# Optimization experiments

Hardware: AMD Instinct MI355X
Metric: run time of the kernel (lower is better)

The kernel has to match this reference:

```python
import jax, jax.numpy as jnp
import numpy as np

MAX_DIST = 10
FP_PENALTY = 2.0


def _min_dist_to(mask, BIG):
    """Per-position distance to the nearest True in mask along axis 1.

    mask: [B, S] bool. Returns int32 [B, S]; BIG where the row has no True.
    Replaces the O(B*S_switch^2) Python loops with two cummax scans.
    """
    B, S = mask.shape
    idx = jnp.arange(S, dtype=jnp.int32)
    def one_side(m):
        last = jax.lax.cummax(jnp.where(m, idx, jnp.int32(-BIG)), axis=1)
        return idx - last  # distance to nearest True at or before each position
    d_fwd = one_side(mask)
    d_bwd = jnp.flip(one_side(jnp.flip(mask, axis=1)), axis=1)
    return jnp.minimum(jnp.minimum(d_fwd, d_bwd), BIG)


def setup_inputs() -> dict:
    key = jax.random.key(0)
    k1, k2 = jax.random.split(key)
    B, S, C = 256, 32768, 3
    logits = jax.random.normal(k1, (B, S, C), dtype=jnp.float32)
    labels = jax.random.randint(k2, (B, S), 0, 3, dtype=jnp.int32)
    distance_weights = jnp.array(
        [1.0, 0.99, 0.95, 0.9, 0.85, 0.8, 0.75, 0.7, 0.65, 0.6, 0.55], jnp.float32)
    class_weights = jnp.array([1.0, 10.0, 10.0], jnp.float32)
    return {"logits": logits, "labels": labels,
            "distance_weights": distance_weights, "class_weights": class_weights}


def reference(logits, labels, distance_weights, class_weights):
    B, S, C = logits.shape
    BIG = 2 * S

    valid = labels != -100
    safe_labels = jnp.where(valid, labels, 0)

    # weighted CE, reduction='none', ignore_index=-100
    logp = jax.nn.log_softmax(logits, axis=-1)
    nll = -jnp.take_along_axis(logp, safe_labels[..., None], axis=-1)[..., 0]
    ce = jnp.where(valid, nll * class_weights[safe_labels], 0.0)

    switch = (labels == 1) | (labels == 2)          # true switch positions
    preds = jnp.argmax(logits, axis=-1)
    pred_switch = (preds == 1) | (preds == 2)       # predicted switch positions

    d_to_true = _min_dist_to(switch, BIG)           # nearest true switch per position
    d_to_pred = _min_dist_to(pred_switch, BIG)      # nearest predicted switch per position

    validf = valid.astype(ce.dtype)

    # proximity bonus at valid predicted-switch positions near a true switch
    n_w = distance_weights.shape[0]
    w = jnp.take(distance_weights, jnp.clip(d_to_true, 0, n_w - 1))
    bonus_mask = pred_switch & valid & (d_to_true <= MAX_DIST)
    bonus = jnp.where(bonus_mask, ce * w * 0.5, 0.0)

    # double CE at valid true switches far from every predicted switch
    # (torch code skips this entirely when the row has no predicted switch)
    has_pred = jnp.any(pred_switch, axis=1, keepdims=True)
    double_mask = switch & valid & has_pred & (d_to_pred > MAX_DIST)
    ce = jnp.where(double_mask, ce * 2.0, ce) - bonus

    masked = ce * validf
    fp = pred_switch.astype(ce.dtype) * (1.0 - switch.astype(ce.dtype)) * validf * FP_PENALTY
    total = masked + fp
    return total.sum() / jnp.maximum(validf.sum(), 1.0)
```

## Files before the change

kernel.cpp:

```cpp
#include <hip/hip_runtime.h>
#include <stdint.h>

#define MAX_DIST 10
#define FP_PENALTY 2.0f
#define CHUNK 4096
#define NT 512
#define PPT (CHUNK / NT)
#define NG 2
#define GP 4
#define NBYTES (CHUNK / 8 + 4)
#define NDW ((NBYTES + 3) / 4)

__global__ __launch_bounds__(NT, 6) void pal_main(
    const float* __restrict__ logits, const int* __restrict__ labels,
    const float* __restrict__ dw, const float* __restrict__ cw,
    double* __restrict__ blk_base, double* __restrict__ blk_extra,
    int* __restrict__ blk_valid, int* __restrict__ blk_haspred,
    int S, int chunks_per_row)
{
    __shared__ unsigned int swb32[NDW];
    __shared__ unsigned int psb32[NDW];
    __shared__ float tbl[12];
    __shared__ float rb[NT / 64], rex[NT / 64];
    __shared__ int rvfp[NT / 64], rp[NT / 64];

    unsigned char* swb = (unsigned char*)swb32;
    unsigned char* psb = (unsigned char*)psb32;

    const int t = threadIdx.x;
    const int wave = t >> 6, lane = t & 63;
    const int blk = blockIdx.x;
    const int row = blk / chunks_per_row;
    const int ck  = blk % chunks_per_row;
    const int s0  = ck * CHUNK;
    const long long rowbase = (long long)row * S;
    const long long pbase = rowbase + s0 + (long long)t * PPT;

    if (t < 12) tbl[t] = (t < 11) ? 0.5f * dw[t] : 0.0f;
    const float cw0 = cw[0], cw1 = cw[1], cw2 = cw[2];

    int4   lb[NG];
    float4 x0[NG], x1[NG], x2[NG];
    #pragma unroll
    for (int g = 0; g < NG; ++g) {
        lb[g] = *(const int4*)(labels + pbase + g * GP);
        const float* lp = logits + (pbase + g * GP) * 3;
        x0[g] = *(const float4*)(lp);
        x1[g] = *(const float4*)(lp + 4);
        x2[g] = *(const float4*)(lp + 8);
    }
    __builtin_amdgcn_sched_barrier(0);

    float ce[PPT];
    unsigned swm = 0u, psm = 0u, vvm = 0u;
    #pragma unroll
    for (int g = 0; g < NG; ++g) {
        const float L[12] = { x0[g].x, x0[g].y, x0[g].z, x0[g].w,
                              x1[g].x, x1[g].y, x1[g].z, x1[g].w,
                              x2[g].x, x2[g].y, x2[g].z, x2[g].w };
        const int lbl4[4] = { lb[g].x, lb[g].y, lb[g].z, lb[g].w };
        #pragma unroll
        for (int i = 0; i < GP; ++i) {
            const int j = g * GP + i;
            const int lbl = lbl4[i];
            const float l0 = L[3*i], l1 = L[3*i+1], l2 = L[3*i+2];

            int pred = 0; float best = l0;
            if (l1 > best) { best = l1; pred = 1; }
            if (l2 > best) { best = l2; pred = 2; }

            const bool valid = (lbl != -100);
            const int sl = valid ? lbl : 0;
            const float a = (pred == 0) ? l1 : l0;
            const float b = (pred == 2) ? l1 : l2;
            const float esum = 1.0f + __expf(a - best) + __expf(b - best);
            const float lse = best + __logf(esum);
            const float lt  = (sl == 0) ? l0 : (sl == 1 ? l1 : l2);
            const float cwv = (sl == 0) ? cw0 : (sl == 1 ? cw1 : cw2);
            ce[j] = valid ? (lse - lt) * cwv : 0.0f;

            swm |= ((lbl == 1) || (lbl == 2)) ? (1u << j) : 0u;
            psm |= (pred != 0) ? (1u << j) : 0u;
            vvm |= valid ? (1u << j) : 0u;
        }
    }
    swb[t + 2] = (unsigned char)swm;
    psb[t + 2] = (unsigned char)psm;
    const int vfp = __popc(vvm) | (__popc(psm & ~swm & vvm) << 16);
    const bool anyp = (psm != 0u);

    if (wave == 0) {
        bool sw = false, ps = false;
        int s = -1;
        if (lane < 10) s = s0 - 10 + lane;
        else if (lane >= 32 && lane < 42) s = s0 + CHUNK + (lane - 32);
        if (s >= 0 && s < S) {
            const long long g = rowbase + s;
            const int lbl = labels[g];
            const float* lp = logits + g * 3;
            const float l0 = lp[0], l1 = lp[1], l2 = lp[2];
            int pred = 0; float best = l0;
            if (l1 > best) { best = l1; pred = 1; }
            if (l2 > best) { best = l2; pred = 2; }
            sw = (lbl == 1) || (lbl == 2);
            ps = (pred == 1) || (pred == 2);
        }
        const unsigned long long bs = __ballot(sw ? 1 : 0);
        const unsigned long long bp = __ballot(ps ? 1 : 0);
        if (lane == 0) {
            *(unsigned short*)&swb[0] = (unsigned short)((bs & 0x3FFull) << 6);
            *(unsigned short*)&psb[0] = (unsigned short)((bp & 0x3FFull) << 6);
            *(unsigned short*)&swb[CHUNK / 8 + 2] = (unsigned short)((bs >> 32) & 0x3FFull);
            *(unsigned short*)&psb[CHUNK / 8 + 2] = (unsigned short)((bp >> 32) & 0x3FFull);
        }
    }
    __syncthreads();

    const int di = t >> 2;
    const int off = ((t & 3) << 3) + 6;
    const unsigned sext = __builtin_amdgcn_alignbit(swb32[di + 1], swb32[di], off);
    const unsigned pext = __builtin_amdgcn_alignbit(psb32[di + 1], psb32[di], off);

    float base_acc = 0.0f, extra_acc = 0.0f;
    #pragma unroll
    for (int j = 0; j < PPT; ++j) {
        const unsigned swin = (sext >> j) & 0x1FFFFFu;
        const unsigned pwin = (pext >> j) & 0x1FFFFFu;

        const bool sw_self = (swin >> 10) & 1u;
        const bool ps_self = (pwin >> 10) & 1u;
        const bool npnear  = (pwin == 0u);

        const unsigned low10 = swin & 0x3FFu;
        const unsigned up10  = (swin >> 11) & 0x3FFu;
        const int ddown = __clz((low10 << 21) | 0x100000u);
        const int dup   = __ffs(up10 | 0x400u);
        int dt = min(ddown, dup);
        dt = sw_self ? 0 : dt;

        const float f = ps_self ? tbl[dt] : 0.0f;
        base_acc += ce[j] * (1.0f - f);
        extra_acc += (sw_self && npnear) ? ce[j] : 0.0f;
    }

    float ba = base_acc, ea = extra_acc; int vf = vfp;
    for (int offr = 32; offr; offr >>= 1) {
        ba += __shfl_down(ba, offr);
        ea += __shfl_down(ea, offr);
        vf += __shfl_down(vf, offr);
    }
    const bool wave_any = __any(anyp ? 1 : 0);
    if (lane == 0) {
        rb[wave] = ba; rex[wave] = ea; rvfp[wave] = vf; rp[wave] = wave_any ? 1 : 0;
    }
    __syncthreads();
    if (t == 0) {
        double bsum = 0.0, esum = 0.0; int vs = 0, fps = 0, ap = 0;
        for (int i = 0; i < NT / 64; ++i) {
            bsum += rb[i]; esum += rex[i];
            vs += rvfp[i] & 0xFFFF; fps += rvfp[i] >> 16; ap |= rp[i];
        }
        blk_base[blk]    = bsum + (double)FP_PENALTY * (double)fps;
        blk_extra[blk]   = esum;
        blk_valid[blk]   = vs;
        blk_haspred[blk] = ap;
    }
}

__global__ __launch_bounds__(256) void pal_finish(
    const double* __restrict__ blk_base, const double* __restrict__ blk_extra,
    const int* __restrict__ blk_valid, const int* __restrict__ blk_haspred,
    int nrows, int chunks_per_row, float* __restrict__ out)
{
    const int t = threadIdx.x;
    double bsum = 0.0, esum = 0.0;
    long long vsum = 0;
    for (int r = t; r < nrows; r += 256) {
        int hp = 0; double e = 0.0;
        for (int c = 0; c < chunks_per_row; ++c) {
            const int i = r * chunks_per_row + c;
            bsum += blk_base[i];
            e    += blk_extra[i];
            hp   |= blk_haspred[i];
            vsum += blk_valid[i];
        }
        if (hp) esum += e;
    }
    __shared__ double sb[256], se[256];
    __shared__ long long sv[256];
    sb[t] = bsum; se[t] = esum; sv[t] = vsum;
    __syncthreads();
    for (int off = 128; off; off >>= 1) {
        if (t < off) { sb[t] += sb[t + off]; se[t] += se[t + off]; sv[t] += sv[t + off]; }
        __syncthreads();
    }
    if (t == 0) {
        const double tot = sb[0] + se[0];
        double denom = (double)sv[0];
        if (denom < 1.0) denom = 1.0;
        out[0] = (float)(tot / denom);
    }
}

extern "C" void kernel_launch(void* const* d_in, const int* in_sizes, int n_in,
                              void* d_out, int out_size, void* d_ws, size_t ws_size,
                              hipStream_t stream)
{
    const float* logits = (const float*)d_in[0];
    const int*   labels = (const int*)d_in[1];
    const float* dw     = (const float*)d_in[2];
    const float* cw     = (const float*)d_in[3];

    const int S = 32768;
    const int Brows = in_sizes[1] / S;
    const int CPR = S / CHUNK;
    const int nblk = Brows * CPR;

    double* blk_base    = (double*)d_ws;
    double* blk_extra   = blk_base + nblk;
    int*    blk_valid   = (int*)(blk_extra + nblk);
    int*    blk_haspred = blk_valid + nblk;

    pal_main<<<nblk, NT, 0, stream>>>(logits, labels, dw, cw,
                                      blk_base, blk_extra, blk_valid, blk_haspred,
                                      S, CPR);
    pal_finish<<<1, 256, 0, stream>>>(blk_base, blk_extra, blk_valid, blk_haspred,
                                      Brows, CPR, (float*)d_out);
}
```

Measured before the change: 34.55 us.

## Fuse final reduction into main kernel via last-block atomic ticket

Drops the separate single-block finish kernel. Each block publishes its partials with atomics and takes a ticket from a global counter, and the last block to finish does the final reduction. This removes one kernel launch and the gap between launches, but adds a memset on the stream and extra shared memory per block for the reduction arrays (about 10KB of doubles and long longs), which may lower occupancy.

```diff
diff --git a/kernel.cpp b/kernel.cpp
--- a/kernel.cpp
+++ b/kernel.cpp
@@ -11,18 +11,22 @@
 #define NBYTES (CHUNK / 8 + 4)
 #define NDW ((NBYTES + 3) / 4)
 
-__global__ __launch_bounds__(NT, 6) void pal_main(
+__global__ __launch_bounds__(NT, 6) void pal_fused(
     const float* __restrict__ logits, const int* __restrict__ labels,
     const float* __restrict__ dw, const float* __restrict__ cw,
-    double* __restrict__ blk_base, double* __restrict__ blk_extra,
-    int* __restrict__ blk_valid, int* __restrict__ blk_haspred,
-    int S, int chunks_per_row)
+    unsigned long long* __restrict__ blk_base, unsigned long long* __restrict__ blk_extra,
+    unsigned int* __restrict__ blk_vh,
+    int* __restrict__ counter, float* __restrict__ out,
+    int S, int chunks_per_row, int nrows)
 {
     __shared__ unsigned int swb32[NDW];
     __shared__ unsigned int psb32[NDW];
     __shared__ float tbl[12];
     __shared__ float rb[NT / 64], rex[NT / 64];
     __shared__ int rvfp[NT / 64], rp[NT / 64];
+    __shared__ int sticket;
+    __shared__ double sb[NT], se[NT];
+    __shared__ long long sv[NT];
 
     unsigned char* swb = (unsigned char*)swb32;
     unsigned char* psb = (unsigned char*)psb32;
@@ -30,6 +34,7 @@
     const int t = threadIdx.x;
     const int wave = t >> 6, lane = t & 63;
     const int blk = blockIdx.x;
+    const int nblk = gridDim.x;
     const int row = blk / chunks_per_row;
     const int ck  = blk % chunks_per_row;
     const int s0  = ck * CHUNK;
@@ -160,38 +165,34 @@
             bsum += rb[i]; esum += rex[i];
             vs += rvfp[i] & 0xFFFF; fps += rvfp[i] >> 16; ap |= rp[i];
         }
-        blk_base[blk]    = bsum + (double)FP_PENALTY * (double)fps;
-        blk_extra[blk]   = esum;
-        blk_valid[blk]   = vs;
-        blk_haspred[blk] = ap;
-    }
-}
-
-__global__ __launch_bounds__(256) void pal_finish(
-    const double* __restrict__ blk_base, const double* __restrict__ blk_extra,
-    const int* __restrict__ blk_valid, const int* __restrict__ blk_haspred,
-    int nrows, int chunks_per_row, float* __restrict__ out)
-{
-    const int t = threadIdx.x;
+        const double bb = bsum + (double)FP_PENALTY * (double)fps;
+        atomicExch(&blk_base[blk], (unsigned long long)__double_as_longlong(bb));
+        atomicExch(&blk_extra[blk], (unsigned long long)__double_as_longlong(esum));
+        atomicExch(&blk_vh[blk], (unsigned)vs | ((unsigned)ap << 31));
+        __threadfence();
+        sticket = atomicAdd(counter, 1);
+    }
+    __syncthreads();
+    if (sticket != nblk - 1) return;
+
     double bsum = 0.0, esum = 0.0;
     long long vsum = 0;
-    for (int r = t; r < nrows; r += 256) {
-        int hp = 0; double e = 0.0;
+    for (int r = t; r < nrows; r += NT) {
+        unsigned hp = 0u; double e = 0.0;
         for (int c = 0; c < chunks_per_row; ++c) {
             const int i = r * chunks_per_row + c;
-            bsum += blk_base[i];
-            e    += blk_extra[i];
-            hp   |= blk_haspred[i];
-            vsum += blk_valid[i];
+            bsum += __longlong_as_double((long long)atomicAdd(&blk_base[i], 0ull));
+            e    += __longlong_as_double((long long)atomicAdd(&blk_extra[i], 0ull));
+            const unsigned vh = atomicAdd(&blk_vh[i], 0u);
+            hp   |= vh >> 31;
+            vsum += (long long)(vh & 0x7FFFFFFFu);
         }
         if (hp) esum += e;
     }
-    __shared__ double sb[256], se[256];
-    __shared__ long long sv[256];
     sb[t] = bsum; se[t] = esum; sv[t] = vsum;
     __syncthreads();
-    for (int off = 128; off; off >>= 1) {
-        if (t < off) { sb[t] += sb[t + off]; se[t] += se[t + off]; sv[t] += sv[t + off]; }
+    for (int offr = NT / 2; offr; offr >>= 1) {
+        if (t < offr) { sb[t] += sb[t + offr]; se[t] += se[t + offr]; sv[t] += sv[t + offr]; }
         __syncthreads();
     }
     if (t == 0) {
@@ -216,14 +217,15 @@
     const int CPR = S / CHUNK;
     const int nblk = Brows * CPR;
 
-    double* blk_base    = (double*)d_ws;
-    double* blk_extra   = blk_base + nblk;
-    int*    blk_valid   = (int*)(blk_extra + nblk);
-    int*    blk_haspred = blk_valid + nblk;
-
-    pal_main<<<nblk, NT, 0, stream>>>(logits, labels, dw, cw,
-                                      blk_base, blk_extra, blk_valid, blk_haspred,
-                                      S, CPR);
-    pal_finish<<<1, 256, 0, stream>>>(blk_base, blk_extra, blk_valid, blk_haspred,
-                                      Brows, CPR, (float*)d_out);
+    unsigned long long* blk_base  = (unsigned long long*)d_ws;
+    unsigned long long* blk_extra = blk_base + nblk;
+    unsigned int*       blk_vh    = (unsigned int*)(blk_extra + nblk);
+    int*                counter   = (int*)(blk_vh + nblk);
+
+    hipMemsetAsync(counter, 0, sizeof(int), stream);
+
+    pal_fused<<<nblk, NT, 0, stream>>>(logits, labels, dw, cw,
+                                       blk_base, blk_extra, blk_vh,
+                                       counter, (float*)d_out,
+                                       S, CPR, Brows);
 }
```

Result: slower. 84.95 us (+145.9%).
